# Optimization experiments

Measured on AMD Instinct MI355X. Metric: run time of the kernel, lower is better.

Reference implementation:

```python
import jax, jax.numpy as jnp
import numpy as np

DIM = 256
HEADS = 8
WS = 8
HID = 512
EPS = 1e-5

def _rel_index(ws):
    coords = np.arange(ws)
    grid = np.stack(np.meshgrid(coords, coords, indexing='ij')).reshape(2, -1)
    rel = (grid[:, :, None] - grid[:, None, :]).transpose(1, 2, 0)
    rel[:, :, 0] += ws - 1
    rel[:, :, 1] += ws - 1
    rel[:, :, 0] *= 2 * ws - 1
    return jnp.asarray(rel.sum(-1))  # [ws*ws, ws*ws] int

REL = _rel_index(WS)

def setup_inputs():
    key = jax.random.key(0)
    ks = iter(jax.random.split(key, 64))
    def w(shape, scale=0.02):
        return jax.random.normal(next(ks), shape, jnp.float32) * scale
    d = {}
    d['spatial'] = jax.random.normal(next(ks), (4, DIM, 128, 128), jnp.float32)
    d['frequency'] = jax.random.normal(next(ks), (4, DIM, 128, 128), jnp.float32)
    for p in ['s', 'f']:
        d[p + '_qw'] = w((DIM, DIM)); d[p + '_qb'] = jnp.zeros((DIM,), jnp.float32)
        d[p + '_kvw'] = w((2 * DIM, DIM)); d[p + '_kvb'] = jnp.zeros((2 * DIM,), jnp.float32)
        d[p + '_rpb'] = w(((2 * WS - 1) ** 2, HEADS))
        d[p + '_pw'] = w((DIM, DIM)); d[p + '_pb'] = jnp.zeros((DIM,), jnp.float32)
    for p in ['ns1', 'nfs', 'ns2', 'nf1', 'nsf', 'nf2']:
        d[p + '_g'] = jnp.ones((DIM,), jnp.float32); d[p + '_b'] = jnp.zeros((DIM,), jnp.float32)
    for p in ['ffns', 'ffnf']:
        d[p + '_w1'] = w((HID, DIM)); d[p + '_b1'] = jnp.zeros((HID,), jnp.float32)
        d[p + '_w2'] = w((DIM, HID)); d[p + '_b2'] = jnp.zeros((DIM,), jnp.float32)
    return d

def _ln(x, g, b):
    m = jnp.mean(x, -1, keepdims=True)
    v = jnp.mean((x - m) ** 2, -1, keepdims=True)
    return (x - m) / jnp.sqrt(v + EPS) * g + b

def _part(x):  # [B,C,H,W] -> [nW*B, WS*WS, C]
    B, C, H, W = x.shape
    x = x.transpose(0, 2, 3, 1).reshape(B, H // WS, WS, W // WS, WS, C)
    return x.transpose(0, 1, 3, 2, 4, 5).reshape(-1, WS * WS, C)

def _unpart(t, B, H, W):  # [nW*B, WS*WS, C] -> [B,C,H,W]
    C = t.shape[-1]
    x = t.reshape(B, H // WS, W // WS, WS, WS, C).transpose(0, 1, 3, 2, 4, 5).reshape(B, H, W, C)
    return x.transpose(0, 3, 1, 2)

def _xattn(qt, st, qw, qb, kvw, kvb, rpb, pw, pb):
    B_, N, C = qt.shape
    hd = C // HEADS
    q = (qt @ qw.T + qb).reshape(B_, N, HEADS, hd).transpose(0, 2, 1, 3) * (hd ** -0.5)
    kv = (st @ kvw.T + kvb).reshape(B_, N, 2, HEADS, hd).transpose(2, 0, 3, 1, 4)
    k, v = kv[0], kv[1]
    bias = rpb[REL.reshape(-1)].reshape(N, N, HEADS).transpose(2, 0, 1)  # [H,N,N]
    attn = jax.nn.softmax(jnp.einsum('bhnd,bhmd->bhnm', q, k) + bias[None], axis=-1)
    out = jnp.einsum('bhnm,bhmd->bhnd', attn, v).transpose(0, 2, 1, 3).reshape(B_, N, C)
    return out @ pw.T + pb

def _mlp(x, w1, b1, w2, b2):
    return jax.nn.gelu(x @ w1.T + b1, approximate=False) @ w2.T + b2

def _forward(spatial, frequency, s_qw, s_qb, s_kvw, s_kvb, s_rpb, s_pw, s_pb,
             f_qw, f_qb, f_kvw, f_kvb, f_rpb, f_pw, f_pb,
             ns1_g, ns1_b, nfs_g, nfs_b, ns2_g, ns2_b, nf1_g, nf1_b, nsf_g, nsf_b, nf2_g, nf2_b,
             ffns_w1, ffns_b1, ffns_w2, ffns_b2, ffnf_w1, ffnf_b1, ffnf_w2, ffnf_b2):
    B, C, H, W = spatial.shape
    s_win = _part(spatial)
    f_win = _part(frequency)
    # direction 1: spatial queries attend to frequency keys/values
    delta_s = _xattn(_ln(s_win, ns1_g, ns1_b), _ln(f_win, nfs_g, nfs_b),
                     s_qw, s_qb, s_kvw, s_kvb, s_rpb, s_pw, s_pb)
    s_win = s_win + delta_s
    s_win = s_win + _mlp(_ln(s_win, ns2_g, ns2_b), ffns_w1, ffns_b1, ffns_w2, ffns_b2)
    spatial_out = _unpart(s_win, B, H, W)
    # _part(spatial_out) == s_win exactly (partition/unpartition are inverses)
    # direction 2: frequency queries attend to updated spatial keys/values
    delta_f = _xattn(_ln(f_win, nf1_g, nf1_b), _ln(s_win, nsf_g, nsf_b),
                     f_qw, f_qb, f_kvw, f_kvb, f_rpb, f_pw, f_pb)
    f_win = f_win + delta_f
    f_win = f_win + _mlp(_ln(f_win, nf2_g, nf2_b), ffnf_w1, ffnf_b1, ffnf_w2, ffnf_b2)
    freq_out = _unpart(f_win, B, H, W)
    return spatial_out, freq_out

def reference(spatial, frequency, s_qw, s_qb, s_kvw, s_kvb, s_rpb, s_pw, s_pb,
              f_qw, f_qb, f_kvw, f_kvb, f_rpb, f_pw, f_pb,
              ns1_g, ns1_b, nfs_g, nfs_b, ns2_g, ns2_b, nf1_g, nf1_b, nsf_g, nsf_b, nf2_g, nf2_b,
              ffns_w1, ffns_b1, ffns_w2, ffns_b2, ffnf_w1, ffnf_b1, ffnf_w2, ffnf_b2):
    return _forward(spatial, frequency, s_qw, s_qb, s_kvw, s_kvb, s_rpb, s_pw, s_pb,
                    f_qw, f_qb, f_kvw, f_kvb, f_rpb, f_pw, f_pb,
                    ns1_g, ns1_b, nfs_g, nfs_b, ns2_g, ns2_b, nf1_g, nf1_b, nsf_g, nsf_b, nf2_g, nf2_b,
                    ffns_w1, ffns_b1, ffns_w2, ffns_b2, ffnf_w1, ffnf_b1, ffnf_w2, ffnf_b2)
```

## Files before the change

### kernel.cpp

```cpp
#include <hip/hip_runtime.h>

typedef unsigned short u16;
typedef unsigned int u32;
typedef unsigned long long u64;
using bf16x8 = __attribute__((ext_vector_type(8))) short;
using f32x4  = __attribute__((ext_vector_type(4))) float;
using u32x4  = __attribute__((ext_vector_type(4))) u32;
using u32x2  = __attribute__((ext_vector_type(2))) u32;

__device__ __forceinline__ float b2f(u16 h) {
    u32 u = ((u32)h) << 16;
    float f;
    __builtin_memcpy(&f, &u, 4);
    return f;
}
__device__ __forceinline__ u16 f2b(float f) {
    u32 u;
    __builtin_memcpy(&u, &f, 4);
    u32 r = (u + 0x7fffu + ((u >> 16) & 1u)) >> 16;
    return (u16)r;
}
__device__ __forceinline__ void gload16(const u16* g, u16* l) {
    __builtin_amdgcn_global_load_lds(
        (const __attribute__((address_space(1))) u32*)g,
        (__attribute__((address_space(3))) u32*)l, 16, 0, 0);
}
__device__ __forceinline__ void hard_barrier() {
    asm volatile("" ::: "memory");
    __builtin_amdgcn_sched_barrier(0);
    __builtin_amdgcn_s_barrier();
    __builtin_amdgcn_sched_barrier(0);
    asm volatile("" ::: "memory");
}

struct WPack { const float* s[10]; };

__global__ __launch_bounds__(256)
void wconv_kernel(WPack p, u16* __restrict__ dst) {
    const int id = blockIdx.x * 256 + threadIdx.x;
    const int e = id * 4;
    const int unit = e >> 16;
    const u64 arrmap = 0x9988766544332110ull;
    const u64 startmap = 0xECB9864310ull;
    const int arr = (int)((arrmap >> (unit * 4)) & 15);
    const int start = (int)((startmap >> (arr * 4)) & 15);
    const int off = e - (start << 16);
    f32x4 v = *(const f32x4*)(p.s[arr] + off);
    u32x2 w;
    w[0] = (u32)f2b(v[0]) | ((u32)f2b(v[1]) << 16);
    w[1] = (u32)f2b(v[2]) | ((u32)f2b(v[3]) << 16);
    *(u32x2*)(dst + e) = w;
}

__global__ __launch_bounds__(256)
void gather_ln_kernel(const float* __restrict__ X, const float* __restrict__ g,
                      const float* __restrict__ bta, u16* __restrict__ lno,
                      u16* __restrict__ raw) {
    __shared__ __align__(16) u16 win[128][264];
    __shared__ float mrs[128][2];
    const int tid = threadIdx.x;
    const int blk2 = blockIdx.x;
    const int b = blk2 >> 7, hb = (blk2 >> 3) & 15, wp = blk2 & 7;
#pragma unroll
    for (int it = 0; it < 8; ++it) {
        const int id = it * 256 + tid;
        const int c = id & 255, y = id >> 8;
        const size_t off =
            (((size_t)(b * 256 + c) * 128) + hb * 8 + y) * 128 + wp * 16;
        f32x4 v0 = *(const f32x4*)(X + off);
        f32x4 v1 = *(const f32x4*)(X + off + 4);
        f32x4 v2 = *(const f32x4*)(X + off + 8);
        f32x4 v3 = *(const f32x4*)(X + off + 12);
#pragma unroll
        for (int x = 0; x < 4; ++x) {
            win[y * 8 + x][c] = f2b(v0[x]);
            win[y * 8 + 4 + x][c] = f2b(v1[x]);
            win[64 + y * 8 + x][c] = f2b(v2[x]);
            win[64 + y * 8 + 4 + x][c] = f2b(v3[x]);
        }
    }
    __syncthreads();
    {
        const int tok = tid >> 1, half = tid & 1;
        float s = 0.f, s2 = 0.f;
#pragma unroll
        for (int i = 0; i < 16; ++i) {
            u32x4 rv = *(const u32x4*)&win[tok][half * 128 + i * 8];
            const u16* pv = (const u16*)&rv;
#pragma unroll
            for (int x = 0; x < 8; ++x) {
                float v = b2f(pv[x]);
                s += v;
                s2 += v * v;
            }
        }
        s += __shfl_xor(s, 1);
        s2 += __shfl_xor(s2, 1);
        const float mean = s * (1.f / 256.f);
        const float var = s2 * (1.f / 256.f) - mean * mean;
        if (!half) {
            mrs[tok][0] = mean;
            mrs[tok][1] = rsqrtf(var + 1e-5f);
        }
    }
    __syncthreads();
    const size_t base = (size_t)((b * 16 + hb) * 16 + wp * 2) * 64 * 256;
#pragma unroll
    for (int it = 0; it < 16; ++it) {
        const int e8 = it * 256 + tid;
        const int tok = e8 >> 5, c0 = (e8 & 31) * 8;
        u32x4 rv = *(const u32x4*)&win[tok][c0];
        if (raw) *(u32x4*)(raw + base + (size_t)e8 * 8) = rv;
        const u16* pv = (const u16*)&rv;
        const float mean = mrs[tok][0], rstd = mrs[tok][1];
        f32x4 g0 = *(const f32x4*)&g[c0];
        f32x4 g1 = *(const f32x4*)&g[c0 + 4];
        f32x4 t0 = *(const f32x4*)&bta[c0];
        f32x4 t1 = *(const f32x4*)&bta[c0 + 4];
        __align__(16) u16 outv[8];
#pragma unroll
        for (int x = 0; x < 4; ++x) {
            outv[x] = f2b((b2f(pv[x]) - mean) * rstd * g0[x] + t0[x]);
            outv[4 + x] = f2b((b2f(pv[4 + x]) - mean) * rstd * g1[x] + t1[x]);
        }
        *(u32x4*)(lno + base + (size_t)e8 * 8) = *(u32x4*)outv;
    }
}

__global__ __launch_bounds__(256)
void ln_kernel(const u16* __restrict__ X, const float* __restrict__ g,
               const float* __restrict__ bta, u16* __restrict__ Y) {
    const int wave = threadIdx.x >> 6, lane = threadIdx.x & 63;
    const size_t tok = (size_t)blockIdx.x * 4 + wave;
    const u16* x = X + tok * 256 + lane * 4;
    u32x2 v = *(const u32x2*)x;
    float f0 = b2f((u16)(v[0] & 0xffff)), f1 = b2f((u16)(v[0] >> 16));
    float f2v = b2f((u16)(v[1] & 0xffff)), f3 = b2f((u16)(v[1] >> 16));
    float s = f0 + f1 + f2v + f3;
    float s2 = f0 * f0 + f1 * f1 + f2v * f2v + f3 * f3;
#pragma unroll
    for (int off = 32; off; off >>= 1) {
        s += __shfl_xor(s, off);
        s2 += __shfl_xor(s2, off);
    }
    const float mean = s * (1.f / 256.f);
    const float var = s2 * (1.f / 256.f) - mean * mean;
    const float rstd = rsqrtf(var + 1e-5f);
    const int c = lane * 4;
    float o0 = (f0 - mean) * rstd * g[c + 0] + bta[c + 0];
    float o1 = (f1 - mean) * rstd * g[c + 1] + bta[c + 1];
    float o2 = (f2v - mean) * rstd * g[c + 2] + bta[c + 2];
    float o3 = (f3 - mean) * rstd * g[c + 3] + bta[c + 3];
    u32 w0 = (u32)f2b(o0) | ((u32)f2b(o1) << 16);
    u32 w1 = (u32)f2b(o2) | ((u32)f2b(o3) << 16);
    u32x2 w;
    w[0] = w0; w[1] = w1;
    *(u32x2*)(Y + tok * 256 + lane * 4) = w;
}

template <int K, int N, int RES, int EPI>
__global__ __launch_bounds__(256)
void gemm_kernel(const u16* __restrict__ A, const u16* __restrict__ Wt,
                 const float* __restrict__ bias, const u16* __restrict__ resw,
                 u16* __restrict__ Cout) {
    constexpr int S = N / 64;
    constexpr int NPH = K / 64;
    __shared__ __align__(16) u16 As[2][64 * 64];
    __shared__ __align__(16) u16 Bs[2][64 * 64];
    const int tid = threadIdx.x;
    const int lane = tid & 63, w = tid >> 6;
    const int cl = lane & 15, g = lane >> 4;
    const int wr = w >> 1, wc = w & 1;
    const int bid = blockIdx.x;
    const int xcd = bid & 7, rest = bid >> 3;
    const int strip = rest % S, mseq = rest / S;
    const int m0 = (xcd * 128 + mseq) * 64;
    const int n0 = strip * 64;
    const int rowg = lane >> 3;
    const int sch = lane & 7;
    f32x4 acc[2][2] = {};

    auto stage = [&](int c) {
        const int buf = c & 1;
#pragma unroll
        for (int it = 0; it < 2; ++it) {
            const int rp = w * 16 + it * 8;
            const int row = rp + rowg;
            const int ch = sch ^ (row & 7);
            gload16(&A[(size_t)(m0 + row) * K + c * 64 + ch * 8],
                    &As[buf][rp * 64]);
            gload16(&Wt[(size_t)(n0 + row) * K + c * 64 + ch * 8],
                    &Bs[buf][rp * 64]);
        }
    };
    stage(0);
    stage(1);
#pragma unroll
    for (int c = 0; c < NPH; ++c) {
        if (c + 1 < NPH)
            asm volatile("s_waitcnt vmcnt(4)" ::: "memory");
        else
            asm volatile("s_waitcnt vmcnt(0)" ::: "memory");
        hard_barrier();
        const u16* Ab = &As[c & 1][0];
        const u16* Bb = &Bs[c & 1][0];
#pragma unroll
        for (int ks = 0; ks < 2; ++ks) {
            const int J = ks * 4 + g;
            bf16x8 af[2], bw[2];
#pragma unroll
            for (int i = 0; i < 2; ++i) {
                const int r = wr * 32 + i * 16 + cl;
                af[i] = *(const bf16x8*)(Ab + r * 64 + (J ^ (r & 7)) * 8);
            }
#pragma unroll
            for (int j = 0; j < 2; ++j) {
                const int r = wc * 32 + j * 16 + cl;
                bw[j] = *(const bf16x8*)(Bb + r * 64 + (J ^ (r & 7)) * 8);
            }
#pragma unroll
            for (int i = 0; i < 2; ++i)
#pragma unroll
                for (int j = 0; j < 2; ++j)
                    acc[i][j] = __builtin_amdgcn_mfma_f32_16x16x32_bf16(
                        af[i], bw[j], acc[i][j], 0, 0, 0);
        }
        asm volatile("s_waitcnt lgkmcnt(0)" ::: "memory");
        hard_barrier();
        if (c + 2 < NPH) stage(c + 2);
    }
    u16 (*Cs)[72] = (u16(*)[72])&As[0][0];
#pragma unroll
    for (int i = 0; i < 2; ++i)
#pragma unroll
        for (int j = 0; j < 2; ++j)
#pragma unroll
            for (int rr = 0; rr < 4; ++rr)
                Cs[wr * 32 + i * 16 + g * 4 + rr][wc * 32 + j * 16 + cl] =
                    f2b(acc[i][j][rr]);
    __syncthreads();
#pragma unroll
    for (int it = 0; it < 2; ++it) {
        const int idx = it * 256 + tid;
        const int row = idx >> 3, ch = idx & 7;
        const int grow = m0 + row, gcol = n0 + ch * 8;
        u32x4 cv = *(const u32x4*)&Cs[row][ch * 8];
        const u16* pc = (const u16*)&cv;
        f32x4 b0 = *(const f32x4*)&bias[gcol];
        f32x4 b1 = *(const f32x4*)&bias[gcol + 4];
        float v[8];
#pragma unroll
        for (int x = 0; x < 4; ++x) {
            v[x] = b2f(pc[x]) + b0[x];
            v[4 + x] = b2f(pc[4 + x]) + b1[x];
        }
        if constexpr (RES == 1) {
            u32x4 rv = *(const u32x4*)&resw[(size_t)grow * N + gcol];
            const u16* pr = (const u16*)&rv;
#pragma unroll
            for (int x = 0; x < 8; ++x) v[x] += b2f(pr[x]);
        }
        if constexpr (EPI == 1)
#pragma unroll
            for (int x = 0; x < 8; ++x)
                v[x] = 0.5f * v[x] * (1.f + erff(v[x] * 0.70710678118654752f));
        u32x4 ov;
#pragma unroll
        for (int x = 0; x < 4; ++x)
            ov[x] = (u32)f2b(v[2 * x]) | ((u32)f2b(v[2 * x + 1]) << 16);
        *(u32x4*)&Cout[(size_t)grow * N + gcol] = ov;
    }
}

__global__ __launch_bounds__(256)
void attn_mfma_kernel(const u16* __restrict__ Q, const u16* __restrict__ KV,
                      const float* __restrict__ rpb, u16* __restrict__ O) {
    __shared__ __align__(16) u16 Pq[4][64][72];
    __shared__ __align__(16) u16 Vt[4][32][72];
    __shared__ float rb[4][228];
    const int w = threadIdx.x >> 6, lane = threadIdx.x & 63;
    const int gw = blockIdx.x * 4 + w;
    const int win = gw >> 3, h = gw & 7;
    const int c = lane & 15, g = lane >> 4;
    for (int i = lane; i < 225; i += 64) rb[w][i] = rpb[i * 8 + h];
    {
        const u16* Vrow = KV + ((size_t)(win * 64 + lane)) * 512 + 256 + h * 32;
        u32x4 vv[4];
#pragma unroll
        for (int ch = 0; ch < 4; ++ch) vv[ch] = *(const u32x4*)(Vrow + ch * 8);
        const u16* pv = (const u16*)vv;
#pragma unroll
        for (int d = 0; d < 32; ++d) Vt[w][d][lane] = pv[d];
    }
    const u16* Qb = Q + ((size_t)win * 64 + c) * 256 + h * 32 + g * 8;
    const u16* Kb = KV + ((size_t)win * 64 + c) * 512 + h * 32 + g * 8;
    bf16x8 qf[4], kf[4];
#pragma unroll
    for (int t = 0; t < 4; ++t) {
        qf[t] = *(const bf16x8*)(Qb + (size_t)t * 16 * 256);
        kf[t] = *(const bf16x8*)(Kb + (size_t)t * 16 * 512);
    }
    f32x4 st[4][4];
#pragma unroll
    for (int kb = 0; kb < 4; ++kb)
#pragma unroll
        for (int qb = 0; qb < 4; ++qb) {
            f32x4 z = {0.f, 0.f, 0.f, 0.f};
            st[kb][qb] = __builtin_amdgcn_mfma_f32_16x16x32_bf16(kf[kb], qf[qb], z, 0, 0, 0);
        }
    __syncthreads();
    const float scale = 0.17677669529663687f;
    const int qy2 = c >> 3, qx = c & 7;
#pragma unroll
    for (int qb = 0; qb < 4; ++qb) {
        float sv[16];
#pragma unroll
        for (int kb = 0; kb < 4; ++kb)
#pragma unroll
            for (int r = 0; r < 4; ++r) {
                const int k = kb * 16 + 4 * g + r;
                const int dy = (qb * 2 + qy2) - (k >> 3) + 7;
                const int dx = qx - (k & 7) + 7;
                sv[kb * 4 + r] = st[kb][qb][r] * scale + rb[w][dy * 15 + dx];
            }
        float mx = sv[0];
#pragma unroll
        for (int j = 1; j < 16; ++j) mx = fmaxf(mx, sv[j]);
        mx = fmaxf(mx, __shfl_xor(mx, 16));
        mx = fmaxf(mx, __shfl_xor(mx, 32));
        float sum = 0.f;
#pragma unroll
        for (int j = 0; j < 16; ++j) {
            sv[j] = __expf(sv[j] - mx);
            sum += sv[j];
        }
        sum += __shfl_xor(sum, 16);
        sum += __shfl_xor(sum, 32);
        const float inv = 1.f / sum;
#pragma unroll
        for (int kb = 0; kb < 4; ++kb) {
            u32x2 pk;
            pk[0] = (u32)f2b(sv[kb * 4 + 0] * inv) | ((u32)f2b(sv[kb * 4 + 1] * inv) << 16);
            pk[1] = (u32)f2b(sv[kb * 4 + 2] * inv) | ((u32)f2b(sv[kb * 4 + 3] * inv) << 16);
            *(u32x2*)&Pq[w][qb * 16 + c][kb * 16 + 4 * g] = pk;
        }
    }
    __syncthreads();
    f32x4 ot[4][2] = {};
#pragma unroll
    for (int ks = 0; ks < 2; ++ks) {
        bf16x8 bfr[2];
#pragma unroll
        for (int db = 0; db < 2; ++db)
            bfr[db] = *(const bf16x8*)&Vt[w][db * 16 + c][ks * 32 + g * 8];
#pragma unroll
        for (int qb = 0; qb < 4; ++qb) {
            bf16x8 af = *(const bf16x8*)&Pq[w][qb * 16 + c][ks * 32 + g * 8];
#pragma unroll
            for (int db = 0; db < 2; ++db)
                ot[qb][db] = __builtin_amdgcn_mfma_f32_16x16x32_bf16(af, bfr[db], ot[qb][db], 0, 0, 0);
        }
    }
    u16* Ob = O + ((size_t)win * 64) * 256 + h * 32;
#pragma unroll
    for (int qb = 0; qb < 4; ++qb)
#pragma unroll
        for (int db = 0; db < 2; ++db)
#pragma unroll
            for (int r = 0; r < 4; ++r)
                Ob[(size_t)(qb * 16 + 4 * g + r) * 256 + db * 16 + c] = f2b(ot[qb][db][r]);
}

__global__ __launch_bounds__(256)
void scatter_kernel(const u16* __restrict__ Wn, float* __restrict__ out) {
    __shared__ __align__(16) u16 win[128][264];
    const int tid = threadIdx.x;
    const int blk2 = blockIdx.x;
    const int b = blk2 >> 7, hb = (blk2 >> 3) & 15, wp = blk2 & 7;
    const size_t base = (size_t)((b * 16 + hb) * 16 + wp * 2) * 64 * 256;
#pragma unroll
    for (int it = 0; it < 16; ++it) {
        const int e8 = it * 256 + tid;
        const int tok = e8 >> 5, c0 = (e8 & 31) * 8;
        *(u32x4*)&win[tok][c0] = *(const u32x4*)(Wn + base + (size_t)e8 * 8);
    }
    __syncthreads();
#pragma unroll
    for (int it = 0; it < 8; ++it) {
        const int id = it * 256 + tid;
        const int c = id & 255, y = id >> 8;
        f32x4 o0, o1, o2, o3;
#pragma unroll
        for (int x = 0; x < 4; ++x) {
            o0[x] = b2f(win[y * 8 + x][c]);
            o1[x] = b2f(win[y * 8 + 4 + x][c]);
            o2[x] = b2f(win[64 + y * 8 + x][c]);
            o3[x] = b2f(win[64 + y * 8 + 4 + x][c]);
        }
        const size_t oo =
            (((size_t)(b * 256 + c) * 128) + hb * 8 + y) * 128 + wp * 16;
        *(f32x4*)(out + oo) = o0;
        *(f32x4*)(out + oo + 4) = o1;
        *(f32x4*)(out + oo + 8) = o2;
        *(f32x4*)(out + oo + 12) = o3;
    }
}

extern "C" void kernel_launch(void* const* d_in, const int* in_sizes, int n_in,
                              void* d_out, int out_size, void* d_ws,
                              size_t ws_size, hipStream_t stream) {
    const float* spatial = (const float*)d_in[0];
    const float* freq    = (const float*)d_in[1];
    const float* s_qw  = (const float*)d_in[2];
    const float* s_qb  = (const float*)d_in[3];
    const float* s_kvw = (const float*)d_in[4];
    const float* s_kvb = (const float*)d_in[5];
    const float* s_rpb = (const float*)d_in[6];
    const float* s_pw  = (const float*)d_in[7];
    const float* s_pb  = (const float*)d_in[8];
    const float* f_qw  = (const float*)d_in[9];
    const float* f_qb  = (const float*)d_in[10];
    const float* f_kvw = (const float*)d_in[11];
    const float* f_kvb = (const float*)d_in[12];
    const float* f_rpb = (const float*)d_in[13];
    const float* f_pw  = (const float*)d_in[14];
    const float* f_pb  = (const float*)d_in[15];
    const float* ns1_g = (const float*)d_in[16];
    const float* ns1_b = (const float*)d_in[17];
    const float* nfs_g = (const float*)d_in[18];
    const float* nfs_b = (const float*)d_in[19];
    const float* ns2_g = (const float*)d_in[20];
    const float* ns2_b = (const float*)d_in[21];
    const float* nf1_g = (const float*)d_in[22];
    const float* nf1_b = (const float*)d_in[23];
    const float* nsf_g = (const float*)d_in[24];
    const float* nsf_b = (const float*)d_in[25];
    const float* nf2_g = (const float*)d_in[26];
    const float* nf2_b = (const float*)d_in[27];
    const float* ffns_w1 = (const float*)d_in[28];
    const float* ffns_b1 = (const float*)d_in[29];
    const float* ffns_w2 = (const float*)d_in[30];
    const float* ffns_b2 = (const float*)d_in[31];
    const float* ffnf_w1 = (const float*)d_in[32];
    const float* ffnf_b1 = (const float*)d_in[33];
    const float* ffnf_w2 = (const float*)d_in[34];
    const float* ffnf_b2 = (const float*)d_in[35];

    float* out = (float*)d_out;
    char* ob = (char*)d_out;
    char* ws = (char*)d_ws;
    const size_t MB32 = (size_t)32 << 20;
    u16* U0  = (u16*)ob;
    u16* U1  = (u16*)(ob + MB32);
    u16* U23 = (u16*)(ob + 2 * MB32);
    u16* W0  = (u16*)ws;
    u16* W1  = (u16*)(ws + MB32);
    u16* WB  = (u16*)(ws + 2 * MB32);
    u16* R0  = (u16*)(ws + 2 * MB32 + (2 << 20));
    u16* R1  = (u16*)(ws + 2 * MB32 + (2 << 20) + MB32);

    const u16* w_sq  = WB;
    const u16* w_skv = WB + 1 * 65536;
    const u16* w_sp  = WB + 3 * 65536;
    const u16* w_sw1 = WB + 4 * 65536;
    const u16* w_sw2 = WB + 6 * 65536;
    const u16* w_fq  = WB + 8 * 65536;
    const u16* w_fkv = WB + 9 * 65536;
    const u16* w_fp  = WB + 11 * 65536;
    const u16* w_fw1 = WB + 12 * 65536;
    const u16* w_fw2 = WB + 14 * 65536;

    WPack wp;
    wp.s[0] = s_qw;  wp.s[1] = s_kvw; wp.s[2] = s_pw;  wp.s[3] = ffns_w1;
    wp.s[4] = ffns_w2; wp.s[5] = f_qw; wp.s[6] = f_kvw; wp.s[7] = f_pw;
    wp.s[8] = ffnf_w1; wp.s[9] = ffnf_w2;

    const dim3 B(256);
    wconv_kernel<<<1024, B, 0, stream>>>(wp, WB);
    gather_ln_kernel<<<512, B, 0, stream>>>(spatial, ns1_g, ns1_b, U0, R0);
    gather_ln_kernel<<<512, B, 0, stream>>>(freq, nfs_g, nfs_b, U1, R1);
    gemm_kernel<256, 512, 0, 0><<<8192, B, 0, stream>>>(
        U1, w_skv, s_kvb, nullptr, U23);
    gemm_kernel<256, 256, 0, 0><<<4096, B, 0, stream>>>(
        U0, w_sq, s_qb, nullptr, U1);
    attn_mfma_kernel<<<2048, B, 0, stream>>>(U1, U23, s_rpb, U0);
    gemm_kernel<256, 256, 1, 0><<<4096, B, 0, stream>>>(
        U0, w_sp, s_pb, R0, U1);
    ln_kernel<<<16384, B, 0, stream>>>(U1, ns2_g, ns2_b, U0);
    gemm_kernel<256, 512, 0, 1><<<8192, B, 0, stream>>>(
        U0, w_sw1, ffns_b1, nullptr, U23);
    gemm_kernel<512, 256, 1, 0><<<4096, B, 0, stream>>>(
        U23, w_sw2, ffns_b2, U1, W0);
    ln_kernel<<<16384, B, 0, stream>>>(W0, nsf_g, nsf_b, U0);
    gemm_kernel<256, 512, 0, 0><<<8192, B, 0, stream>>>(
        U0, w_fkv, f_kvb, nullptr, U23);
    ln_kernel<<<16384, B, 0, stream>>>(R1, nf1_g, nf1_b, U0);
    gemm_kernel<256, 256, 0, 0><<<4096, B, 0, stream>>>(
        U0, w_fq, f_qb, nullptr, U1);
    attn_mfma_kernel<<<2048, B, 0, stream>>>(U1, U23, f_rpb, U0);
    gemm_kernel<256, 256, 1, 0><<<4096, B, 0, stream>>>(
        U0, w_fp, f_pb, R1, W1);
    ln_kernel<<<16384, B, 0, stream>>>(W1, nf2_g, nf2_b, U0);
    gemm_kernel<256, 512, 0, 1><<<8192, B, 0, stream>>>(
        U0, w_fw1, ffnf_b1, nullptr, U23);
    scatter_kernel<<<512, B, 0, stream>>>(W0, out);
    gemm_kernel<512, 256, 1, 0><<<4096, B, 0, stream>>>(
        U23, w_fw2, ffnf_b2, W1, W0);
    scatter_kernel<<<512, B, 0, stream>>>(W0, out + 16777216);
}
```

Baseline: 584.0 us.

## Fold LayerNorm into following GEMMs via gamma-scaled weights and epilogue correction

LayerNorm gamma is folded into the bf16 weight conversion, and per-output-column G = W·gamma and B = W·beta are precomputed. The GEMMs now consume raw activations, and the epilogue applies rstd*acc - mean*rstd*G + B using per-token mean/rstd. That per-token data comes from lightweight stats kernels in place of full LN-write kernels. This removes the bf16 writes and re-reads of normalized tensors. The cost is extra epilogue loads and a numerical risk: the mean subtraction now happens after the bf16 matmul, which can cancel badly when the mean is large.

```diff
diff --git a/kernel.cpp b/kernel.cpp
--- a/kernel.cpp
+++ b/kernel.cpp
@@ -33,7 +33,7 @@
     asm volatile("" ::: "memory");
 }
 
-struct WPack { const float* s[10]; };
+struct WPack { const float* s[10]; const float* gn[10]; };
 
 __global__ __launch_bounds__(256)
 void wconv_kernel(WPack p, u16* __restrict__ dst) {
@@ -46,18 +46,49 @@
     const int start = (int)((startmap >> (arr * 4)) & 15);
     const int off = e - (start << 16);
     f32x4 v = *(const f32x4*)(p.s[arr] + off);
+    const float* gp = p.gn[arr];
+    if (gp) {
+        f32x4 gv = *(const f32x4*)(gp + (off & 255));
+        v[0] *= gv[0]; v[1] *= gv[1]; v[2] *= gv[2]; v[3] *= gv[3];
+    }
     u32x2 w;
     w[0] = (u32)f2b(v[0]) | ((u32)f2b(v[1]) << 16);
     w[1] = (u32)f2b(v[2]) | ((u32)f2b(v[3]) << 16);
     *(u32x2*)(dst + e) = w;
 }
 
-__global__ __launch_bounds__(256)
-void gather_ln_kernel(const float* __restrict__ X, const float* __restrict__ g,
-                      const float* __restrict__ bta, u16* __restrict__ lno,
-                      u16* __restrict__ raw) {
+struct GBPack { const float* w[6]; const float* g[6]; const float* bt[6];
+                int nstart[7]; };
+
+__global__ __launch_bounds__(256)
+void gb_kernel(GBPack p, float* __restrict__ G, float* __restrict__ Bv) {
+    const int wid = blockIdx.x * 4 + (threadIdx.x >> 6);
+    const int lane = threadIdx.x & 63;
+    int i = 0;
+    while (i < 5 && wid >= p.nstart[i + 1]) ++i;
+    const int nl = wid - p.nstart[i];
+    const float* wr = p.w[i] + (size_t)nl * 256;
+    const float* gr = p.g[i];
+    const float* br = p.bt[i];
+    float s = 0.f, t = 0.f;
+#pragma unroll
+    for (int x = 0; x < 4; ++x) {
+        const float wv = wr[lane * 4 + x];
+        s += gr[lane * 4 + x] * wv;
+        t += br[lane * 4 + x] * wv;
+    }
+#pragma unroll
+    for (int o = 32; o; o >>= 1) {
+        s += __shfl_xor(s, o);
+        t += __shfl_xor(t, o);
+    }
+    if (!lane) { G[wid] = s; Bv[wid] = t; }
+}
+
+__global__ __launch_bounds__(256)
+void gather_stats_kernel(const float* __restrict__ X, u16* __restrict__ raw,
+                         float* __restrict__ SS) {
     __shared__ __align__(16) u16 win[128][264];
-    __shared__ float mrs[128][2];
     const int tid = threadIdx.x;
     const int blk2 = blockIdx.x;
     const int b = blk2 >> 7, hb = (blk2 >> 3) & 15, wp = blk2 & 7;
@@ -80,6 +111,7 @@
         }
     }
     __syncthreads();
+    const size_t btok = (size_t)((b * 16 + hb) * 16 + wp * 2) * 64;
     {
         const int tok = tid >> 1, half = tid & 1;
         float s = 0.f, s2 = 0.f;
@@ -99,41 +131,24 @@
         const float mean = s * (1.f / 256.f);
         const float var = s2 * (1.f / 256.f) - mean * mean;
         if (!half) {
-            mrs[tok][0] = mean;
-            mrs[tok][1] = rsqrtf(var + 1e-5f);
-        }
-    }
-    __syncthreads();
-    const size_t base = (size_t)((b * 16 + hb) * 16 + wp * 2) * 64 * 256;
+            SS[(btok + tok) * 2] = mean;
+            SS[(btok + tok) * 2 + 1] = rsqrtf(var + 1e-5f);
+        }
+    }
+    const size_t base = btok * 256;
 #pragma unroll
     for (int it = 0; it < 16; ++it) {
         const int e8 = it * 256 + tid;
         const int tok = e8 >> 5, c0 = (e8 & 31) * 8;
-        u32x4 rv = *(const u32x4*)&win[tok][c0];
-        if (raw) *(u32x4*)(raw + base + (size_t)e8 * 8) = rv;
-        const u16* pv = (const u16*)&rv;
-        const float mean = mrs[tok][0], rstd = mrs[tok][1];
-        f32x4 g0 = *(const f32x4*)&g[c0];
-        f32x4 g1 = *(const f32x4*)&g[c0 + 4];
-        f32x4 t0 = *(const f32x4*)&bta[c0];
-        f32x4 t1 = *(const f32x4*)&bta[c0 + 4];
-        __align__(16) u16 outv[8];
-#pragma unroll
-        for (int x = 0; x < 4; ++x) {
-            outv[x] = f2b((b2f(pv[x]) - mean) * rstd * g0[x] + t0[x]);
-            outv[4 + x] = f2b((b2f(pv[4 + x]) - mean) * rstd * g1[x] + t1[x]);
-        }
-        *(u32x4*)(lno + base + (size_t)e8 * 8) = *(u32x4*)outv;
-    }
-}
-
-__global__ __launch_bounds__(256)
-void ln_kernel(const u16* __restrict__ X, const float* __restrict__ g,
-               const float* __restrict__ bta, u16* __restrict__ Y) {
+        *(u32x4*)(raw + base + (size_t)e8 * 8) = *(const u32x4*)&win[tok][c0];
+    }
+}
+
+__global__ __launch_bounds__(256)
+void stats_kernel(const u16* __restrict__ X, float* __restrict__ SS) {
     const int wave = threadIdx.x >> 6, lane = threadIdx.x & 63;
     const size_t tok = (size_t)blockIdx.x * 4 + wave;
-    const u16* x = X + tok * 256 + lane * 4;
-    u32x2 v = *(const u32x2*)x;
+    u32x2 v = *(const u32x2*)(X + tok * 256 + lane * 4);
     float f0 = b2f((u16)(v[0] & 0xffff)), f1 = b2f((u16)(v[0] >> 16));
     float f2v = b2f((u16)(v[1] & 0xffff)), f3 = b2f((u16)(v[1] >> 16));
     float s = f0 + f1 + f2v + f3;
@@ -143,26 +158,20 @@
         s += __shfl_xor(s, off);
         s2 += __shfl_xor(s2, off);
     }
-    const float mean = s * (1.f / 256.f);
-    const float var = s2 * (1.f / 256.f) - mean * mean;
-    const float rstd = rsqrtf(var + 1e-5f);
-    const int c = lane * 4;
-    float o0 = (f0 - mean) * rstd * g[c + 0] + bta[c + 0];
-    float o1 = (f1 - mean) * rstd * g[c + 1] + bta[c + 1];
-    float o2 = (f2v - mean) * rstd * g[c + 2] + bta[c + 2];
-    float o3 = (f3 - mean) * rstd * g[c + 3] + bta[c + 3];
-    u32 w0 = (u32)f2b(o0) | ((u32)f2b(o1) << 16);
-    u32 w1 = (u32)f2b(o2) | ((u32)f2b(o3) << 16);
-    u32x2 w;
-    w[0] = w0; w[1] = w1;
-    *(u32x2*)(Y + tok * 256 + lane * 4) = w;
-}
-
-template <int K, int N, int RES, int EPI>
+    if (!lane) {
+        const float mean = s * (1.f / 256.f);
+        const float var = s2 * (1.f / 256.f) - mean * mean;
+        SS[tok * 2] = mean;
+        SS[tok * 2 + 1] = rsqrtf(var + 1e-5f);
+    }
+}
+
+template <int K, int N, int LNE, int RES, int EPI>
 __global__ __launch_bounds__(256)
 void gemm_kernel(const u16* __restrict__ A, const u16* __restrict__ Wt,
-                 const float* __restrict__ bias, const u16* __restrict__ resw,
-                 u16* __restrict__ Cout) {
+                 const float* __restrict__ bias, const float* __restrict__ stats,
+                 const float* __restrict__ Gv, const float* __restrict__ Bv,
+                 const u16* __restrict__ resw, u16* __restrict__ Cout) {
     constexpr int S = N / 64;
     constexpr int NPH = K / 64;
     __shared__ __align__(16) u16 As[2][64 * 64];
@@ -249,10 +258,25 @@
         f32x4 b0 = *(const f32x4*)&bias[gcol];
         f32x4 b1 = *(const f32x4*)&bias[gcol + 4];
         float v[8];
-#pragma unroll
-        for (int x = 0; x < 4; ++x) {
-            v[x] = b2f(pc[x]) + b0[x];
-            v[4 + x] = b2f(pc[4 + x]) + b1[x];
+        if constexpr (LNE) {
+            const float mean = stats[2 * (size_t)grow];
+            const float rstd = stats[2 * (size_t)grow + 1];
+            const float mr = mean * rstd;
+            f32x4 G0 = *(const f32x4*)&Gv[gcol];
+            f32x4 G1 = *(const f32x4*)&Gv[gcol + 4];
+            f32x4 B0 = *(const f32x4*)&Bv[gcol];
+            f32x4 B1 = *(const f32x4*)&Bv[gcol + 4];
+#pragma unroll
+            for (int x = 0; x < 4; ++x) {
+                v[x] = rstd * b2f(pc[x]) - mr * G0[x] + B0[x] + b0[x];
+                v[4 + x] = rstd * b2f(pc[4 + x]) - mr * G1[x] + B1[x] + b1[x];
+            }
+        } else {
+#pragma unroll
+            for (int x = 0; x < 4; ++x) {
+                v[x] = b2f(pc[x]) + b0[x];
+                v[4 + x] = b2f(pc[4 + x]) + b1[x];
+            }
         }
         if constexpr (RES == 1) {
             u32x4 rv = *(const u32x4*)&resw[(size_t)grow * N + gcol];
@@ -458,6 +482,14 @@
     u16* WB  = (u16*)(ws + 2 * MB32);
     u16* R0  = (u16*)(ws + 2 * MB32 + (2 << 20));
     u16* R1  = (u16*)(ws + 2 * MB32 + (2 << 20) + MB32);
+    char* SSB = ws + 2 * MB32 + (2 << 20) + 2 * MB32;
+    float* SS0 = (float*)SSB;
+    float* SS1 = (float*)(SSB + (512 << 10));
+    float* SS2 = (float*)(SSB + (1024 << 10));
+    float* SS3 = (float*)(SSB + (1536 << 10));
+    float* SS4 = (float*)(SSB + (2048 << 10));
+    float* Gv  = (float*)(SSB + (2560 << 10));
+    float* Bv  = Gv + 2560;
 
     const u16* w_sq  = WB;
     const u16* w_skv = WB + 1 * 65536;
@@ -471,40 +503,64 @@
     const u16* w_fw2 = WB + 14 * 65536;
 
     WPack wp;
-    wp.s[0] = s_qw;  wp.s[1] = s_kvw; wp.s[2] = s_pw;  wp.s[3] = ffns_w1;
-    wp.s[4] = ffns_w2; wp.s[5] = f_qw; wp.s[6] = f_kvw; wp.s[7] = f_pw;
-    wp.s[8] = ffnf_w1; wp.s[9] = ffnf_w2;
+    wp.s[0] = s_qw;    wp.gn[0] = ns1_g;
+    wp.s[1] = s_kvw;   wp.gn[1] = nfs_g;
+    wp.s[2] = s_pw;    wp.gn[2] = nullptr;
+    wp.s[3] = ffns_w1; wp.gn[3] = ns2_g;
+    wp.s[4] = ffns_w2; wp.gn[4] = nullptr;
+    wp.s[5] = f_qw;    wp.gn[5] = nf1_g;
+    wp.s[6] = f_kvw;   wp.gn[6] = nsf_g;
+    wp.s[7] = f_pw;    wp.gn[7] = nullptr;
+    wp.s[8] = ffnf_w1; wp.gn[8] = nf2_g;
+    wp.s[9] = ffnf_w2; wp.gn[9] = nullptr;
+
+    GBPack gp;
+    gp.w[0] = s_qw;    gp.g[0] = ns1_g; gp.bt[0] = ns1_b;
+    gp.w[1] = s_kvw;   gp.g[1] = nfs_g; gp.bt[1] = nfs_b;
+    gp.w[2] = ffns_w1; gp.g[2] = ns2_g; gp.bt[2] = ns2_b;
+    gp.w[3] = f_qw;    gp.g[3] = nf1_g; gp.bt[3] = nf1_b;
+    gp.w[4] = f_kvw;   gp.g[4] = nsf_g; gp.bt[4] = nsf_b;
+    gp.w[5] = ffnf_w1; gp.g[5] = nf2_g; gp.bt[5] = nf2_b;
+    gp.nstart[0] = 0;    gp.nstart[1] = 256;  gp.nstart[2] = 768;
+    gp.nstart[3] = 1280; gp.nstart[4] = 1536; gp.nstart[5] = 2048;
+    gp.nstart[6] = 2560;
+    const float* G_sq  = Gv + 0;    const float* B_sq  = Bv + 0;
+    const float* G_skv = Gv + 256;  const float* B_skv = Bv + 256;
+    const float* G_sw1 = Gv + 768;  const float* B_sw1 = Bv + 768;
+    const float* G_fq  = Gv + 1280; const float* B_fq  = Bv + 1280;
+    const float* G_fkv = Gv + 1536; const float* B_fkv = Bv + 1536;
+    const float* G_fw1 = Gv + 2048; const float* B_fw1 = Bv + 2048;
 
     const dim3 B(256);
     wconv_kernel<<<1024, B, 0, stream>>>(wp, WB);
-    gather_ln_kernel<<<512, B, 0, stream>>>(spatial, ns1_g, ns1_b, U0, R0);
-    gather_ln_kernel<<<512, B, 0, stream>>>(freq, nfs_g, nfs_b, U1, R1);
-    gemm_kernel<256, 512, 0, 0><<<8192, B, 0, stream>>>(
-        U1, w_skv, s_kvb, nullptr, U23);
-    gemm_kernel<256, 256, 0, 0><<<4096, B, 0, stream>>>(
-        U0, w_sq, s_qb, nullptr, U1);
+    gb_kernel<<<640, B, 0, stream>>>(gp, Gv, Bv);
+    gather_stats_kernel<<<512, B, 0, stream>>>(spatial, R0, SS0);
+    gather_stats_kernel<<<512, B, 0, stream>>>(freq, R1, SS1);
+    gemm_kernel<256, 512, 1, 0, 0><<<8192, B, 0, stream>>>(
+        R1, w_skv, s_kvb, SS1, G_skv, B_skv, nullptr, U23);
+    gemm_kernel<256, 256, 1, 0, 0><<<4096, B, 0, stream>>>(
+        R0, w_sq, s_qb, SS0, G_sq, B_sq, nullptr, U1);
     attn_mfma_kernel<<<2048, B, 0, stream>>>(U1, U23, s_rpb, U0);
-    gemm_kernel<256, 256, 1, 0><<<4096, B, 0, stream>>>(
-        U0, w_sp, s_pb, R0, U1);
-    ln_kernel<<<16384, B, 0, stream>>>(U1, ns2_g, ns2_b, U0);
-    gemm_kernel<256, 512, 0, 1><<<8192, B, 0, stream>>>(
-        U0, w_sw1, ffns_b1, nullptr, U23);
-    gemm_kernel<512, 256, 1, 0><<<4096, B, 0, stream>>>(
-        U23, w_sw2, ffns_b2, U1, W0);
-    ln_kernel<<<16384, B, 0, stream>>>(W0, nsf_g, nsf_b, U0);
-    gemm_kernel<256, 512, 0, 0><<<8192, B, 0, stream>>>(
-        U0, w_fkv, f_kvb, nullptr, U23);
-    ln_kernel<<<16384, B, 0, stream>>>(R1, nf1_g, nf1_b, U0);
-    gemm_kernel<256, 256, 0, 0><<<4096, B, 0, stream>>>(
-        U0, w_fq, f_qb, nullptr, U1);
+    gemm_kernel<256, 256, 0, 1, 0><<<4096, B, 0, stream>>>(
+        U0, w_sp, s_pb, nullptr, nullptr, nullptr, R0, U1);
+    stats_kernel<<<16384, B, 0, stream>>>(U1, SS2);
+    gemm_kernel<256, 512, 1, 0, 1><<<8192, B, 0, stream>>>(
+        U1, w_sw1, ffns_b1, SS2, G_sw1, B_sw1, nullptr, U23);
+    gemm_kernel<512, 256, 0, 1, 0><<<4096, B, 0, stream>>>(
+        U23, w_sw2, ffns_b2, nullptr, nullptr, nullptr, U1, W0);
+    stats_kernel<<<16384, B, 0, stream>>>(W0, SS3);
+    gemm_kernel<256, 512, 1, 0, 0><<<8192, B, 0, stream>>>(
+        W0, w_fkv, f_kvb, SS3, G_fkv, B_fkv, nullptr, U23);
+    gemm_kernel<256, 256, 1, 0, 0><<<4096, B, 0, stream>>>(
+        R1, w_fq, f_qb, SS1, G_fq, B_fq, nullptr, U1);
     attn_mfma_kernel<<<2048, B, 0, stream>>>(U1, U23, f_rpb, U0);
-    gemm_kernel<256, 256, 1, 0><<<4096, B, 0, stream>>>(
-        U0, w_fp, f_pb, R1, W1);
-    ln_kernel<<<16384, B, 0, stream>>>(W1, nf2_g, nf2_b, U0);
-    gemm_kernel<256, 512, 0, 1><<<8192, B, 0, stream>>>(
-        U0, w_fw1, ffnf_b1, nullptr, U23);
+    gemm_kernel<256, 256, 0, 1, 0><<<4096, B, 0, stream>>>(
+        U0, w_fp, f_pb, nullptr, nullptr, nullptr, R1, W1);
+    stats_kernel<<<16384, B, 0, stream>>>(W1, SS4);
+    gemm_kernel<256, 512, 1, 0, 1><<<8192, B, 0, stream>>>(
+        W1, w_fw1, ffnf_b1, SS4, G_fw1, B_fw1, nullptr, U23);
     scatter_kernel<<<512, B, 0, stream>>>(W0, out);
-    gemm_kernel<512, 256, 1, 0><<<4096, B, 0, stream>>>(
-        U23, w_fw2, ffnf_b2, W1, W0);
+    gemm_kernel<512, 256, 0, 1, 0><<<4096, B, 0, stream>>>(
+        U23, w_fw2, ffnf_b2, nullptr, nullptr, nullptr, W1, W0);
     scatter_kernel<<<512, B, 0, stream>>>(W0, out + 16777216);
 }
```

After: 562.8 us. -3.6%, faster.
